# Kernel optimization log

Hardware: AMD Instinct MI355X
Metric: run time of the kernel (lower is better)

The kernel has to match this reference:

```python
import jax, jax.numpy as jnp
import numpy as np

VOCAB = 50257
NUM_TAGS = 50
EMB_DIM = 128
CTX = 2
N_TOKENS = 262144


def setup_inputs() -> dict:
    key = jax.random.key(0)
    k1, k2, k3, k4 = jax.random.split(key, 4)
    tokens = jax.random.randint(k1, (N_TOKENS,), 0, VOCAB, dtype=jnp.int64 if jax.config.jax_enable_x64 else jnp.int32)
    emb_table = jax.random.normal(k2, (VOCAB, EMB_DIM), dtype=jnp.float32)
    W = jax.random.normal(k3, (NUM_TAGS, EMB_DIM * (1 + 2 * CTX)), dtype=jnp.float32) * 0.05
    b = jax.random.normal(k4, (NUM_TAGS,), dtype=jnp.float32) * 0.05
    return {"tokens": tokens, "emb_table": emb_table, "W": W, "b": b}


def reference(tokens, emb_table, W, b):
    # [N, D] embedding gather
    emb = emb_table[tokens]
    n = emb.shape[0]
    # zero-pad CTX positions on each side (matches torch.zeros_like padding)
    padded = jnp.pad(emb, ((CTX, CTX), (0, 0)))
    # sliding window concat: [N, (2*CTX+1)*D] via 2*CTX+1 shifted views
    windows = jnp.concatenate([padded[i:i + n] for i in range(2 * CTX + 1)], axis=-1)
    logits = windows @ W.T + b  # [N, num_tags]
    log_probs = jax.nn.log_softmax(logits, axis=-1)
    return log_probs
```

## Files before the change

kernel.cpp:

```cpp
#include <hip/hip_runtime.h>
#include <hip/hip_bf16.h>

#define VOCAB 50257
#define NTAGS 50
#define EMB   128
#define NTOK  262144
#define KD    640
#define WPAD  64

#define TAGP  64
#define NZ    320
#define ZROWS 50304

#define TOK   56
#define RWS   60
#define CHR   40
#define NCHUNK (RWS*CHR)
#define NITER  ((NCHUNK+63)/64)

typedef __attribute__((ext_vector_type(4))) float f32x4;
typedef __attribute__((ext_vector_type(8))) short bf16x8;

__device__ __forceinline__ ushort f2bf(float f) {
    union { float f; unsigned u; } v; v.f = f;
    unsigned u = v.u;
    return (ushort)((u + 0x7fffu + ((u >> 16) & 1u)) >> 16);
}

__device__ __forceinline__ void gload_lds16(const void* g, void* l) {
    __builtin_amdgcn_global_load_lds(
        (const __attribute__((address_space(1))) unsigned*)g,
        (__attribute__((address_space(3))) unsigned*)l, 16, 0, 0);
}


__global__ __launch_bounds__(256)
void zt_k(const float* __restrict__ emb, const float* __restrict__ W,
          ushort* __restrict__ ZT) {
    __shared__ __align__(16) char wlds[NZ * EMB * 2];

    const int tid  = threadIdx.x;
    const int lane = tid & 63;
    const int wave = tid >> 6;
    const int c = lane & 15, q = lane >> 4;
    const int vb = blockIdx.x * 128;

    #pragma unroll
    for (int it = 0; it < 20; ++it) {
        int g = it * 256 + tid;
        int n = g >> 4, j = g & 15;
        int tg = n & 63, p = n >> 6;
        bf16x8 val = (bf16x8){0,0,0,0,0,0,0,0};
        if (tg < NTAGS) {
            const float* wp = W + tg * KD + p * EMB + j * 8;
            f32x4 lo = *(const f32x4*)wp;
            f32x4 hi = *(const f32x4*)(wp + 4);
            val[0]=(short)f2bf(lo[0]); val[1]=(short)f2bf(lo[1]);
            val[2]=(short)f2bf(lo[2]); val[3]=(short)f2bf(lo[3]);
            val[4]=(short)f2bf(hi[0]); val[5]=(short)f2bf(hi[1]);
            val[6]=(short)f2bf(hi[2]); val[7]=(short)f2bf(hi[3]);
        }
        *(bf16x8*)(wlds + n * 256 + ((j ^ (n & 7)) << 4)) = val;
    }

    bf16x8 A[2][4];
    #pragma unroll
    for (int mt = 0; mt < 2; ++mt) {
        int row = vb + wave * 32 + mt * 16 + c;
        bool ok = row < VOCAB;
        const float* rp = emb + (size_t)(ok ? row : 0) * EMB;
        #pragma unroll
        for (int kk = 0; kk < 4; ++kk) {
            f32x4 lo = {0,0,0,0}, hi = {0,0,0,0};
            if (ok) {
                lo = *(const f32x4*)(rp + kk * 32 + q * 8);
                hi = *(const f32x4*)(rp + kk * 32 + q * 8 + 4);
            }
            bf16x8 a;
            a[0]=(short)f2bf(lo[0]); a[1]=(short)f2bf(lo[1]);
            a[2]=(short)f2bf(lo[2]); a[3]=(short)f2bf(lo[3]);
            a[4]=(short)f2bf(hi[0]); a[5]=(short)f2bf(hi[1]);
            a[6]=(short)f2bf(hi[2]); a[7]=(short)f2bf(hi[3]);
            A[mt][kk] = a;
        }
    }
    __syncthreads();

    #pragma unroll
    for (int ng = 0; ng < 5; ++ng) {
        bf16x8 B[4][4];
        #pragma unroll
        for (int nt = 0; nt < 4; ++nt) {
            #pragma unroll
            for (int kk = 0; kk < 4; ++kk) {
                int r  = ng * 64 + nt * 16 + c;
                int ph = (kk * 4 + q) ^ (c & 7);
                B[nt][kk] = *(const bf16x8*)(wlds + r * 256 + ph * 16);
            }
        }
        #pragma unroll
        for (int mt = 0; mt < 2; ++mt) {
            f32x4 acc[4];
            #pragma unroll
            for (int nt = 0; nt < 4; ++nt) acc[nt] = (f32x4){0.f,0.f,0.f,0.f};
            #pragma unroll
            for (int kk = 0; kk < 4; ++kk)
                #pragma unroll
                for (int nt = 0; nt < 4; ++nt)
                    acc[nt] = __builtin_amdgcn_mfma_f32_16x16x32_bf16(
                        A[mt][kk], B[nt][kk], acc[nt], 0, 0, 0);
            #pragma unroll
            for (int nt = 0; nt < 4; ++nt)
                #pragma unroll
                for (int j = 0; j < 4; ++j)
                    ZT[(size_t)(vb + wave * 32 + mt * 16 + q * 4 + j) * NZ
                       + ng * 64 + nt * 16 + c] = f2bf(acc[nt][j]);
        }
    }
}

__global__ __launch_bounds__(64, 1)
void tag_k(const int* __restrict__ tokens, const ushort* __restrict__ ZT,
           const float* __restrict__ bias, float* __restrict__ out) {
    __shared__ __align__(16) char smem[RWS * 640 + RWS * 4];
    int* ids = (int*)(smem + RWS * 640);

    const int l  = threadIdx.x;
    const int bb = blockIdx.x * TOK;

    {
        int t = bb - 2 + l;
        if (l < RWS) ids[l] = ((unsigned)t < NTOK) ? tokens[t] : VOCAB;
    }
    __syncthreads();

    int tk[NITER];
    #pragma unroll
    for (int w = 0; w < NITER; ++w) {
        int g = w * 64 + l;
        int r = (g < NCHUNK) ? (g / CHR) : 0;
        tk[w] = ids[r];
    }

    #pragma unroll
    for (int w = 0; w < NITER; ++w) {
        int g = w * 64 + l;
        if (g < NCHUNK) {
            int r  = g / CHR;
            int ch = g - r * CHR;
            int i  = ch & 7, p = ch >> 3;
            const char* src = (const char*)ZT + (size_t)tk[w] * 640
                              + p * 128 + ((i ^ (r & 7)) << 4);
            gload_lds16(src, smem + w * 1024);
        }
    }
    __syncthreads();

    float acc[56];
    #pragma unroll
    for (int g = 0; g < 12; ++g) {
        float4 b4 = *(const float4*)(bias + g * 4);
        acc[g*4+0] = b4.x; acc[g*4+1] = b4.y; acc[g*4+2] = b4.z; acc[g*4+3] = b4.w;
    }
    acc[48] = bias[48]; acc[49] = bias[49];
    #pragma unroll
    for (int j = 50; j < 56; ++j) acc[j] = 0.f;

    {
        const int le = (l < TOK) ? l : (TOK - 1);
        bf16x8 v[5][7];
        #pragma unroll
        for (int p = 0; p < 5; ++p) {
            const int rp = le + p;
            const char* rb = smem + rp * 640;
            const int rx = (rp & 7) << 4;
            #pragma unroll
            for (int j = 0; j < 7; ++j)
                v[p][j] = *(const bf16x8*)(rb + p * 128 + ((j << 4) ^ rx));
        }
        #pragma unroll
        for (int p = 0; p < 5; ++p)
            #pragma unroll
            for (int j = 0; j < 7; ++j)
                #pragma unroll
                for (int e = 0; e < 8; ++e) {
                    unsigned u = (unsigned)(ushort)v[p][j][e] << 16;
                    acc[j*8+e] += __uint_as_float(u);
                }
    }

    float m = acc[0];
    #pragma unroll
    for (int j = 1; j < NTAGS; ++j) m = fmaxf(m, acc[j]);
    float s = 0.f;
    #pragma unroll
    for (int j = 0; j < NTAGS; ++j) s += __expf(acc[j] - m);
    const float L = m + __logf(s);

    __syncthreads();
    if (l < TOK) {
        #pragma unroll
        for (int k = 0; k < 25; ++k) {
            float2 st = { acc[2*k] - L, acc[2*k+1] - L };
            *(float2*)(smem + (size_t)l * 200 + k * 8) = st;
        }
    }
    __syncthreads();
    const int nvalid = (NTOK - bb < TOK) ? (NTOK - bb) : TOK;
    const int nbytes = nvalid * 200;
    char* ob = (char*)out + (size_t)bb * 200;
    #pragma unroll
    for (int w = 0; w < 11; ++w) {
        int off = w * 1024 + l * 16;
        if (off < nbytes) {
            f32x4 d = *(const f32x4*)(smem + off);
            *(f32x4*)(ob + off) = d;
        }
    }
}

__global__ void fb_conv_k(const float* __restrict__ emb, const float* __restrict__ W,
                          ushort* __restrict__ embb, ushort* __restrict__ wb) {
    const int etotal = (VOCAB + 1) * EMB;
    int idx = (blockIdx.x * blockDim.x + threadIdx.x) * 4;
    if (idx < etotal) {
        float4 v = {0.f, 0.f, 0.f, 0.f};
        if (idx < VOCAB * EMB) v = *(const float4*)(emb + idx);
        ushort4 o = { f2bf(v.x), f2bf(v.y), f2bf(v.z), f2bf(v.w) };
        *(ushort4*)(embb + idx) = o;
    } else {
        int wi = idx - etotal;
        if (wi < WPAD * KD) {
            #pragma unroll
            for (int k = 0; k < 4; ++k) {
                int j = wi + k;
                int tag = j / KD;
                wb[j] = f2bf(tag < NTAGS ? W[j] : 0.f);
            }
        }
    }
}

__global__ __launch_bounds__(64, 2)
void fb_tag_k(const int* __restrict__ tokens, const ushort* __restrict__ embb,
              const ushort* __restrict__ Wb, const float* __restrict__ bias,
              float* __restrict__ out) {
    __shared__ ushort smem[68 * EMB];
    const int lane = threadIdx.x & 63;
    const int c = lane & 15;
    const int q = lane >> 4;
    const int bb = blockIdx.x * 64;
    const int rsub = lane >> 4;

    int tokid[17];
    #pragma unroll
    for (int g = 0; g < 17; ++g) {
        int t = bb - 2 + g * 4 + rsub;
        tokid[g] = (t >= 0 && t < NTOK) ? tokens[t] : VOCAB;
    }
    const ushort* bp[4];
    #pragma unroll
    for (int nt = 0; nt < 4; ++nt)
        bp[nt] = Wb + (nt * 16 + c) * KD + q * 8;
    bf16x8 Bb[4][4];
    #pragma unroll
    for (int s = 0; s < 4; ++s)
        #pragma unroll
        for (int nt = 0; nt < 4; ++nt)
            Bb[s][nt] = *(const bf16x8*)(bp[nt] + (s >> 2) * 128 + (s & 3) * 32);
    float bv[4];
    #pragma unroll
    for (int nt = 0; nt < 4; ++nt) {
        int tag = nt * 16 + c;
        bv[nt] = bias[tag < NTAGS ? tag : NTAGS - 1];
    }
    {
        const int pc = lane & 15;
        #pragma unroll
        for (int g = 0; g < 17; ++g) {
            int i = g * 4 + rsub;
            int sc = pc ^ (i & 7);
            gload_lds16(embb + (size_t)tokid[g] * EMB + sc * 8, (char*)smem + g * 1024);
        }
    }
    __syncthreads();

    f32x4 acc[4][4];
    #pragma unroll
    for (int mt = 0; mt < 4; ++mt)
        #pragma unroll
        for (int nt = 0; nt < 4; ++nt)
            acc[mt][nt] = (f32x4){0.f, 0.f, 0.f, 0.f};
    bf16x8 Ab[2][4];
    #pragma unroll
    for (int s = 0; s < 2; ++s) {
        int p = s >> 2, kk = s & 3;
        int ch = (4 * kk + q) ^ ((c + p) & 7);
        const char* ab = (const char*)smem + (c + p) * 256 + ch * 16;
        #pragma unroll
        for (int mt = 0; mt < 4; ++mt)
            Ab[s][mt] = *(const bf16x8*)(ab + mt * 4096);
    }
    #pragma unroll
    for (int s = 0; s < 20; ++s) {
        __builtin_amdgcn_s_setprio(1);
        #pragma unroll
        for (int mt = 0; mt < 4; ++mt)
            #pragma unroll
            for (int nt = 0; nt < 4; ++nt)
                acc[mt][nt] = __builtin_amdgcn_mfma_f32_16x16x32_bf16(
                    Ab[s & 1][mt], Bb[s & 3][nt], acc[mt][nt], 0, 0, 0);
        __builtin_amdgcn_s_setprio(0);
        if (s + 4 < 20) {
            const int tt = s + 4, p = tt >> 2, kk = tt & 3;
            #pragma unroll
            for (int nt = 0; nt < 4; ++nt)
                Bb[s & 3][nt] = *(const bf16x8*)(bp[nt] + p * 128 + kk * 32);
        }
        if (s + 2 < 20) {
            const int tt = s + 2, p = tt >> 2, kk = tt & 3;
            int ch = (4 * kk + q) ^ ((c + p) & 7);
            const char* ab = (const char*)smem + (c + p) * 256 + ch * 16;
            #pragma unroll
            for (int mt = 0; mt < 4; ++mt)
                Ab[s & 1][mt] = *(const bf16x8*)(ab + mt * 4096);
        }
    }
    #pragma unroll
    for (int mt = 0; mt < 4; ++mt) {
        #pragma unroll
        for (int j = 0; j < 4; ++j) {
            const int row = bb + mt * 16 + q * 4 + j;
            float x[4];
            float m = -1e30f;
            #pragma unroll
            for (int nt = 0; nt < 4; ++nt) {
                float xv = acc[mt][nt][j] + bv[nt];
                x[nt] = xv;
                if (nt * 16 + c < NTAGS) m = fmaxf(m, xv);
            }
            #pragma unroll
            for (int mask = 8; mask >= 1; mask >>= 1)
                m = fmaxf(m, __shfl_xor(m, mask));
            float s = 0.f;
            #pragma unroll
            for (int nt = 0; nt < 4; ++nt)
                if (nt * 16 + c < NTAGS) s += __expf(x[nt] - m);
            #pragma unroll
            for (int mask = 8; mask >= 1; mask >>= 1)
                s += __shfl_xor(s, mask);
            const float L = m + __logf(s);
            #pragma unroll
            for (int nt = 0; nt < 4; ++nt) {
                int tag = nt * 16 + c;
                if (tag < NTAGS) out[row * NTAGS + tag] = x[nt] - L;
            }
        }
    }
}

extern "C" void kernel_launch(void* const* d_in, const int* in_sizes, int n_in,
                              void* d_out, int out_size, void* d_ws, size_t ws_size,
                              hipStream_t stream) {
    const int*   tokens = (const int*)d_in[0];
    const float* emb    = (const float*)d_in[1];
    const float* W      = (const float*)d_in[2];
    const float* b      = (const float*)d_in[3];
    float* out = (float*)d_out;

    const size_t NEED = (size_t)ZROWS * NZ * 2ull;
    if (ws_size >= NEED) {
        ushort* ZT = (ushort*)d_ws;
        zt_k<<<ZROWS / 128, 256, 0, stream>>>(emb, W, ZT);
        tag_k<<<(NTOK + TOK - 1) / TOK, 64, 0, stream>>>(tokens, ZT, b, out);
    } else {
        ushort* embb = (ushort*)d_ws;
        ushort* Wb   = embb + (size_t)(VOCAB + 1) * EMB;
        const int etotal = (VOCAB + 1) * EMB;
        const int total4 = (etotal + WPAD * KD) / 4;
        fb_conv_k<<<(total4 + 255) / 256, 256, 0, stream>>>(emb, W, embb, Wb);
        fb_tag_k<<<NTOK / 64, 64, 0, stream>>>(tokens, embb, Wb, b, out);
    }
}
```

Measured before the change: 68.07 us.

## Swap MFMA operands for vectorized ZT stores and shrink per-block token count

The vocab-projection kernel swaps the MFMA operand roles so W tiles form the M side and embedding rows the N side. Each lane then holds four consecutive tag outputs for one vocab row, which lets it write them as a single ushort4 store instead of scattered 2-byte stores. Separately, the tagging kernel handles 24 tokens per block instead of 56, with shared memory and the output copy loop resized to match. This gives more, smaller blocks for better occupancy and load balance, at the cost of more redundant halo-row gathers per token.

```diff
diff --git a/kernel.cpp b/kernel.cpp
--- a/kernel.cpp
+++ b/kernel.cpp
@@ -12,8 +12,8 @@
 #define NZ    320
 #define ZROWS 50304
 
-#define TOK   56
-#define RWS   60
+#define TOK   24
+#define RWS   28
 #define CHR   40
 #define NCHUNK (RWS*CHR)
 #define NITER  ((NCHUNK+63)/64)
@@ -63,10 +63,10 @@
         *(bf16x8*)(wlds + n * 256 + ((j ^ (n & 7)) << 4)) = val;
     }
 
-    bf16x8 A[2][4];
-    #pragma unroll
-    for (int mt = 0; mt < 2; ++mt) {
-        int row = vb + wave * 32 + mt * 16 + c;
+    bf16x8 E[2][4];
+    #pragma unroll
+    for (int nv = 0; nv < 2; ++nv) {
+        int row = vb + wave * 32 + nv * 16 + c;
         bool ok = row < VOCAB;
         const float* rp = emb + (size_t)(ok ? row : 0) * EMB;
         #pragma unroll
@@ -81,40 +81,46 @@
             a[2]=(short)f2bf(lo[2]); a[3]=(short)f2bf(lo[3]);
             a[4]=(short)f2bf(hi[0]); a[5]=(short)f2bf(hi[1]);
             a[6]=(short)f2bf(hi[2]); a[7]=(short)f2bf(hi[3]);
-            A[mt][kk] = a;
+            E[nv][kk] = a;
         }
     }
     __syncthreads();
 
     #pragma unroll
     for (int ng = 0; ng < 5; ++ng) {
-        bf16x8 B[4][4];
-        #pragma unroll
-        for (int nt = 0; nt < 4; ++nt) {
+        bf16x8 Wf[4][4];
+        #pragma unroll
+        for (int mtag = 0; mtag < 4; ++mtag) {
             #pragma unroll
             for (int kk = 0; kk < 4; ++kk) {
-                int r  = ng * 64 + nt * 16 + c;
+                int r  = ng * 64 + mtag * 16 + c;
                 int ph = (kk * 4 + q) ^ (c & 7);
-                B[nt][kk] = *(const bf16x8*)(wlds + r * 256 + ph * 16);
-            }
-        }
-        #pragma unroll
-        for (int mt = 0; mt < 2; ++mt) {
-            f32x4 acc[4];
-            #pragma unroll
-            for (int nt = 0; nt < 4; ++nt) acc[nt] = (f32x4){0.f,0.f,0.f,0.f};
-            #pragma unroll
-            for (int kk = 0; kk < 4; ++kk)
+                Wf[mtag][kk] = *(const bf16x8*)(wlds + r * 256 + ph * 16);
+            }
+        }
+        f32x4 acc[4][2];
+        #pragma unroll
+        for (int mtag = 0; mtag < 4; ++mtag)
+            #pragma unroll
+            for (int nv = 0; nv < 2; ++nv)
+                acc[mtag][nv] = (f32x4){0.f,0.f,0.f,0.f};
+        #pragma unroll
+        for (int kk = 0; kk < 4; ++kk)
+            #pragma unroll
+            for (int mtag = 0; mtag < 4; ++mtag)
                 #pragma unroll
-                for (int nt = 0; nt < 4; ++nt)
-                    acc[nt] = __builtin_amdgcn_mfma_f32_16x16x32_bf16(
-                        A[mt][kk], B[nt][kk], acc[nt], 0, 0, 0);
-            #pragma unroll
-            for (int nt = 0; nt < 4; ++nt)
-                #pragma unroll
-                for (int j = 0; j < 4; ++j)
-                    ZT[(size_t)(vb + wave * 32 + mt * 16 + q * 4 + j) * NZ
-                       + ng * 64 + nt * 16 + c] = f2bf(acc[nt][j]);
+                for (int nv = 0; nv < 2; ++nv)
+                    acc[mtag][nv] = __builtin_amdgcn_mfma_f32_16x16x32_bf16(
+                        Wf[mtag][kk], E[nv][kk], acc[mtag][nv], 0, 0, 0);
+        #pragma unroll
+        for (int nv = 0; nv < 2; ++nv) {
+            const size_t row = (size_t)(vb + wave * 32 + nv * 16 + c);
+            #pragma unroll
+            for (int mtag = 0; mtag < 4; ++mtag) {
+                ushort4 o = { f2bf(acc[mtag][nv][0]), f2bf(acc[mtag][nv][1]),
+                              f2bf(acc[mtag][nv][2]), f2bf(acc[mtag][nv][3]) };
+                *(ushort4*)(ZT + row * NZ + ng * 64 + mtag * 16 + q * 4) = o;
+            }
         }
     }
 }
@@ -122,7 +128,7 @@
 __global__ __launch_bounds__(64, 1)
 void tag_k(const int* __restrict__ tokens, const ushort* __restrict__ ZT,
            const float* __restrict__ bias, float* __restrict__ out) {
-    __shared__ __align__(16) char smem[RWS * 640 + RWS * 4];
+    __shared__ __align__(16) char smem[RWS * 640 + 128];
     int* ids = (int*)(smem + RWS * 640);
 
     const int l  = threadIdx.x;
@@ -210,7 +216,7 @@
     const int nbytes = nvalid * 200;
     char* ob = (char*)out + (size_t)bb * 200;
     #pragma unroll
-    for (int w = 0; w < 11; ++w) {
+    for (int w = 0; w < 5; ++w) {
         int off = w * 1024 + l * 16;
         if (off < nbytes) {
             f32x4 d = *(const f32x4*)(smem + off);
```

New measurement: 68.86 us. About the same (+1.1%).
